# Performance work log

Measured on AMD Instinct MI355X. Metric: run time of the kernel, lower is better.

## Reference

```python
import jax, jax.numpy as jnp
import numpy as np

B, L, D = 8, 1024, 768
H, W, Dd = 16, 16, 4          # token grid, H*W*Dd == L
N, R, K = 16, 48, 4           # d_state, dt_rank, d_conv
EPS = 1e-5


def _physical_pos_embed(batch_params, has_velocity):
    # physical coords [B, L, 3]: (distance, angle, velocity/time)
    h_idx = jnp.arange(H, dtype=jnp.float32)[None, :, None, None]
    w_idx = jnp.arange(W, dtype=jnp.float32)[None, None, :, None]
    d_idx = jnp.arange(Dd, dtype=jnp.float32)[None, None, None, :]
    rres = batch_params[:, 0][:, None, None, None]
    ares = batch_params[:, 1][:, None, None, None]
    vres = batch_params[:, 2][:, None, None, None]
    zero = jnp.zeros((1, H, W, Dd), jnp.float32)
    dist = h_idx * rres + zero
    ang = (w_idx - W / 2) * ares + zero
    vel = jnp.where(has_velocity[:, None, None, None],
                    (d_idx - Dd / 2) * vres, d_idx * vres) + zero
    coords = jnp.stack([dist, ang, vel], axis=-1).reshape(B, L, 3)
    mx = coords.max(axis=1, keepdims=True)
    mn = coords.min(axis=1, keepdims=True)
    rng = mx - mn
    rng = jnp.where(rng > 0, rng, jnp.ones_like(rng))
    coords = (coords - mn) / rng
    # sincos embed: D/3 = 256 dims per coord (even -> pure sin/cos)
    fdim = D // 3
    omega = jnp.arange(fdim // 2, dtype=jnp.float32) / (fdim / 2.0)
    omega = 1.0 / (10000.0 ** omega)                      # [128]
    out = jnp.einsum('blc,f->blcf', coords, omega)        # [B,L,3,128]
    emb = jnp.concatenate([jnp.sin(out), jnp.cos(out)], axis=-1)  # [B,L,3,256]
    return emb.reshape(B, L, D)


def _rmsnorm(x, w):
    return x * jax.lax.rsqrt(jnp.mean(x * x, axis=-1, keepdims=True) + EPS) * w


def _mamba(h, in_proj_w, in_proj_b, conv_w, conv_b, x_proj_w,
           dt_proj_w, dt_proj_b, A_log, D_param, out_proj_w, out_proj_b):
    xz = h @ in_proj_w.T + in_proj_b                      # [B,L,2D]
    x_in, z = xz[..., :D], xz[..., D:]
    # causal depthwise conv1d, kernel K
    xp = jnp.pad(x_in, ((0, 0), (K - 1, 0), (0, 0)))
    x_conv = sum(xp[:, k:k + L, :] * conv_w[:, 0, k] for k in range(K))
    x_conv = jax.nn.silu(x_conv + conv_b)
    x_dbl = x_conv @ x_proj_w.T                           # [B,L,R+2N]
    dt, Bm, Cm = x_dbl[..., :R], x_dbl[..., R:R + N], x_dbl[..., R + N:]
    dt = jax.nn.softplus(dt @ dt_proj_w.T + dt_proj_b)    # [B,L,D]
    A = -jnp.exp(A_log)                                   # [D,N]
    dA = jnp.exp(dt[..., None] * A)                       # [B,L,D,N]
    dBx = dt[..., None] * Bm[:, :, None, :] * x_conv[..., None]

    def step(hst, inp):
        dA_t, dBx_t, C_t = inp
        hst = dA_t * hst + dBx_t                          # [B,D,N]
        y_t = jnp.einsum('bdn,bn->bd', hst, C_t)
        return hst, y_t

    h0 = jnp.zeros((B, D, N), x_in.dtype)
    _, ys = jax.lax.scan(step, h0, (dA.transpose(1, 0, 2, 3),
                                    dBx.transpose(1, 0, 2, 3),
                                    Cm.transpose(1, 0, 2)))
    y = ys.transpose(1, 0, 2) + D_param * x_conv          # [B,L,D]
    y = y * jax.nn.silu(z)
    return y @ out_proj_w.T + out_proj_b


def reference(x, batch_params, has_velocity, norm_w, in_proj_w, in_proj_b,
              conv_w, conv_b, x_proj_w, dt_proj_w, dt_proj_b, A_log,
              D_param, out_proj_w, out_proj_b):
    pos = _physical_pos_embed(batch_params, has_velocity)
    residual = x + pos                                    # ARBlock residual
    hidden = _rmsnorm(residual, norm_w)
    hidden = _mamba(hidden, in_proj_w, in_proj_b, conv_w, conv_b, x_proj_w,
                    dt_proj_w, dt_proj_b, A_log, D_param,
                    out_proj_w, out_proj_b)
    return hidden + residual


def setup_inputs():
    key = jax.random.key(0)
    ks = jax.random.split(key, 12)
    s = 0.02
    return {
        'x': jax.random.normal(ks[0], (B, L, D), jnp.float32),
        'batch_params': jax.random.uniform(ks[1], (B, 4), jnp.float32, 0.01, 1.0),
        'has_velocity': jax.random.randint(ks[2], (B,), 0, 2) > 0,
        'norm_w': jnp.ones((D,), jnp.float32),
        'in_proj_w': jax.random.normal(ks[3], (2 * D, D), jnp.float32) * s,
        'in_proj_b': jnp.zeros((2 * D,), jnp.float32),
        'conv_w': jax.random.normal(ks[4], (D, 1, K), jnp.float32) * 0.3,
        'conv_b': jnp.zeros((D,), jnp.float32),
        'x_proj_w': jax.random.normal(ks[5], (R + 2 * N, D), jnp.float32) * s,
        'dt_proj_w': jax.random.normal(ks[6], (D, R), jnp.float32) * s,
        'dt_proj_b': jax.random.normal(ks[7], (D,), jnp.float32) * 0.1,
        'A_log': jnp.log(jax.random.uniform(ks[8], (D, N), jnp.float32, 1.0, 16.0)),
        'D_param': jnp.ones((D,), jnp.float32),
        'out_proj_w': jax.random.normal(ks[9], (D, D), jnp.float32) * s,
        'out_proj_b': jnp.zeros((D,), jnp.float32),
    }
```

## Files before the change

### kernel.cpp

```cpp
#include <hip/hip_runtime.h>
#include <math.h>

#define BB 8
#define LL 1024
#define DD 768
#define NNs 16
#define RR 48

typedef __attribute__((ext_vector_type(8))) short bf16x8;
typedef __attribute__((ext_vector_type(4))) float f32x4;

__device__ __forceinline__ float silu_f(float v) { return v / (1.0f + __expf(-v)); }

__device__ __forceinline__ short f2bf(float f) {
    union { float f; unsigned u; } v; v.f = f;
    unsigned r = (v.u + 0x7fffu + ((v.u >> 16) & 1u)) >> 16;
    return (short)r;
}

__device__ __forceinline__ float exp2_fast(float x) {
    float r;
    asm("v_exp_f32 %0, %1" : "=v"(r) : "v"(x));
    return r;
}

__device__ __forceinline__ void async16(const void* g, void* l) {
    __builtin_amdgcn_global_load_lds((const __attribute__((address_space(1))) void*)g,
                                     (__attribute__((address_space(3))) void*)l,
                                     16, 0, 0);
}

__global__ __launch_bounds__(256) void k_cvt2(const float* __restrict__ s1,
                                              short* __restrict__ d1, int n1,
                                              const float* __restrict__ s2,
                                              short* __restrict__ d2, int n2) {
    int i = blockIdx.x * 256 + threadIdx.x;
    if (i < n1) {
        float4 v = ((const float4*)s1)[i];
        short4 o = { f2bf(v.x), f2bf(v.y), f2bf(v.z), f2bf(v.w) };
        ((short4*)d1)[i] = o;
    } else {
        int j = i - n1;
        if (j < n2) {
            float4 v = ((const float4*)s2)[j];
            short4 o = { f2bf(v.x), f2bf(v.y), f2bf(v.z), f2bf(v.w) };
            ((short4*)d2)[j] = o;
        }
    }
}

__global__ __launch_bounds__(256) void k_pos_rms(const float* __restrict__ x,
                                                 const float* __restrict__ norm_w,
                                                 float* __restrict__ res,
                                                 short* __restrict__ hidb) {
    int row = blockIdx.x;
    int l = row & (LL - 1);
    int d3 = l & 3;
    int w = (l >> 2) & 15;
    int h = l >> 6;
    float coord[3] = { h * (1.0f / 15.0f), w * (1.0f / 15.0f), d3 * (1.0f / 3.0f) };
    const float LOG1E4 = 9.210340371976184f;
    int t = threadIdx.x;
    float r[3];
    float s = 0.0f;
#pragma unroll
    for (int i = 0; i < 3; i++) {
        int j = t + i * 256;
        int c = j >> 8;
        int fp = j & 255;
        int f = fp & 127;
        float omega = __expf(-(f * (1.0f / 128.0f)) * LOG1E4);
        float arg = coord[c] * omega;
        float pv = (fp < 128) ? __sinf(arg) : __cosf(arg);
        float rv = x[(size_t)row * DD + j] + pv;
        r[i] = rv;
        s += rv * rv;
    }
#pragma unroll
    for (int off = 32; off; off >>= 1) s += __shfl_xor(s, off, 64);
    __shared__ float ls[4];
    if ((t & 63) == 0) ls[t >> 6] = s;
    __syncthreads();
    s = ls[0] + ls[1] + ls[2] + ls[3];
    float rs = rsqrtf(s * (1.0f / DD) + 1e-5f);
#pragma unroll
    for (int i = 0; i < 3; i++) {
        int j = t + i * 256;
        res[(size_t)row * DD + j] = r[i];
        hidb[(size_t)row * DD + j] = f2bf(r[i] * rs * norm_w[j]);
    }
}

template <int EPI, bool AF32>
__global__ __launch_bounds__(256) void gemm_mfma(const void* __restrict__ Ap,
                                                 const short* __restrict__ Bw,
                                                 int Kd,
                                                 const float* __restrict__ bias,
                                                 const float* __restrict__ resid,
                                                 float* __restrict__ C0,
                                                 float* __restrict__ C1) {
    __shared__ short As[4096];
    __shared__ short Bs[4096];
    int m0 = blockIdx.y * 128;
    int n0 = blockIdx.x * 128;
    int tid = threadIdx.x;
    int lane = tid & 63, wave = tid >> 6;
    int q = lane >> 4, r = lane & 15;
    int wm = wave >> 1, wn = wave & 1;

    const size_t Kb = (size_t)Kd * 2;
    const char* gB0 = (const char*)Bw + (size_t)(n0 + wave * 16 + r) * Kb + q * 16;
    const char* gB1 = gB0 + 64 * Kb;
    char* lB0 = (char*)Bs + wave * 1024;
    char* lB1 = lB0 + 4096;
    const char* gA0 = nullptr; const char* gA1 = nullptr;
    char* lA0 = nullptr; char* lA1 = nullptr;
    if (!AF32) {
        gA0 = (const char*)Ap + (size_t)(m0 + wave * 16 + r) * Kb + q * 16;
        gA1 = gA0 + 64 * Kb;
        lA0 = (char*)As + wave * 1024;
        lA1 = lA0 + 4096;
    }

    f32x4 acc[4][4] = {};

    for (int k0 = 0; k0 < Kd; k0 += 32) {
        if (AF32) {
            const float* Af = (const float*)Ap;
#pragma unroll
            for (int p = 0; p < 2; p++) {
                int m = m0 + (p * 4 + wave) * 16 + r;
                const float* src = Af + (size_t)m * Kd + k0 + q * 8;
                float4 v0 = *(const float4*)src;
                float4 v1 = *(const float4*)(src + 4);
                bf16x8 pk;
                pk[0] = f2bf(v0.x); pk[1] = f2bf(v0.y);
                pk[2] = f2bf(v0.z); pk[3] = f2bf(v0.w);
                pk[4] = f2bf(v1.x); pk[5] = f2bf(v1.y);
                pk[6] = f2bf(v1.z); pk[7] = f2bf(v1.w);
                *(bf16x8*)&As[p * 2048 + wave * 512 + lane * 8] = pk;
            }
        } else {
            async16(gA0, lA0); async16(gA1, lA1);
            gA0 += 64; gA1 += 64;
        }
        async16(gB0, lB0); async16(gB1, lB1);
        gB0 += 64; gB1 += 64;
        __syncthreads();
        bf16x8 af[4], bf[4];
#pragma unroll
        for (int a = 0; a < 4; a++)
            af[a] = *(const bf16x8*)&As[((wm * 4 + a) * 64 + q * 16 + r) * 8];
#pragma unroll
        for (int b = 0; b < 4; b++)
            bf[b] = *(const bf16x8*)&Bs[((wn * 4 + b) * 64 + q * 16 + r) * 8];
#pragma unroll
        for (int a = 0; a < 4; a++)
#pragma unroll
            for (int b = 0; b < 4; b++)
                acc[a][b] = __builtin_amdgcn_mfma_f32_16x16x32_bf16(
                    af[a], bf[b], acc[a][b], 0, 0, 0);
        __syncthreads();
    }

#pragma unroll
    for (int a = 0; a < 4; a++) {
        int mrow = m0 + (wm * 4 + a) * 16 + q * 4;
#pragma unroll
        for (int b = 0; b < 4; b++) {
            int ncol = n0 + (wn * 4 + b) * 16 + r;
            float bb = bias[ncol];
            if (EPI == 1) {
                float* dst = (ncol < DD) ? (C0 + (size_t)mrow * DD + ncol)
                                         : (C1 + (size_t)mrow * DD + (ncol - DD));
#pragma unroll
                for (int e = 0; e < 4; e++)
                    dst[(size_t)e * DD] = acc[a][b][e] + bb;
            } else {
#pragma unroll
                for (int e = 0; e < 4; e++) {
                    size_t idx = (size_t)(mrow + e) * DD + ncol;
                    C0[idx] = acc[a][b][e] + bb + resid[idx];
                }
            }
        }
    }
}

template <int MODE>
__global__ __launch_bounds__(256) void gemm_nt(const float* __restrict__ A, int lda,
                                               const float* __restrict__ Bw, int ldb,
                                               int N, int Kd,
                                               const float* __restrict__ bias,
                                               float* __restrict__ C0, int ldc) {
    __shared__ __align__(16) float As[16][68];
    __shared__ __align__(16) float Bs[16][68];
    int m0 = blockIdx.y * 64;
    int n0 = blockIdx.x * 64;
    int t = threadIdx.x;
    int tx = t & 15, ty = t >> 4;
    int ar = t >> 2;
    int ak = (t & 3) * 4;
    float acc[4][4] = {};
    for (int k0 = 0; k0 < Kd; k0 += 16) {
        float4 av = *(const float4*)(A + (size_t)(m0 + ar) * lda + k0 + ak);
        int brow = n0 + ar;
        if (brow >= N) brow = N - 1;
        float4 bv = *(const float4*)(Bw + (size_t)brow * ldb + k0 + ak);
        As[ak + 0][ar] = av.x; As[ak + 1][ar] = av.y;
        As[ak + 2][ar] = av.z; As[ak + 3][ar] = av.w;
        Bs[ak + 0][ar] = bv.x; Bs[ak + 1][ar] = bv.y;
        Bs[ak + 2][ar] = bv.z; Bs[ak + 3][ar] = bv.w;
        __syncthreads();
#pragma unroll
        for (int kk = 0; kk < 16; kk++) {
            float4 a4 = *(const float4*)&As[kk][ty * 4];
            float4 b4 = *(const float4*)&Bs[kk][tx * 4];
            float aa[4] = { a4.x, a4.y, a4.z, a4.w };
            float bb[4] = { b4.x, b4.y, b4.z, b4.w };
#pragma unroll
            for (int i = 0; i < 4; i++)
#pragma unroll
                for (int j = 0; j < 4; j++) acc[i][j] += aa[i] * bb[j];
        }
        __syncthreads();
    }
    if (MODE == 0) {
#pragma unroll
        for (int i = 0; i < 4; i++) {
            int m = m0 + ty * 4 + i;
#pragma unroll
            for (int j = 0; j < 4; j++) {
                int n = n0 + tx * 4 + j;
                if (n < N) C0[(size_t)m * ldc + n] = acc[i][j];
            }
        }
    } else {
        float4 bi = *(const float4*)(bias + n0 + tx * 4);
        float bl[4] = { bi.x, bi.y, bi.z, bi.w };
#pragma unroll
        for (int i = 0; i < 4; i++) {
            int m = m0 + ty * 4 + i;
            float v[4];
#pragma unroll
            for (int j = 0; j < 4; j++) {
                float u = acc[i][j] + bl[j];
                v[j] = (u > 20.0f) ? u : log1pf(__expf(u));
            }
            float4 o = { v[0], v[1], v[2], v[3] };
            *(float4*)(C0 + (size_t)m * DD + n0 + tx * 4) = o;
        }
    }
}

__global__ __launch_bounds__(256) void k_conv(const float* __restrict__ xin,
                                              const float* __restrict__ cw,
                                              const float* __restrict__ cb,
                                              float* __restrict__ xc) {
    size_t gid = (size_t)blockIdx.x * 256 + threadIdx.x;
    int d = (int)(gid % DD);
    int bt = (int)(gid / DD);
    int tt = bt & (LL - 1);
    float4 w = ((const float4*)cw)[d];
    const float* p = xin + (size_t)bt * DD + d;
    float acc = cb[d];
    if (tt >= 3) acc += p[-3 * DD] * w.x;
    if (tt >= 2) acc += p[-2 * DD] * w.y;
    if (tt >= 1) acc += p[-1 * DD] * w.z;
    acc += p[0] * w.w;
    xc[gid] = silu_f(acc);
}

__global__ __launch_bounds__(256, 3) void k_scan(const float* __restrict__ dtf,
                                                 const float* __restrict__ xc,
                                                 const float* __restrict__ xdbl,
                                                 const float* __restrict__ A_log,
                                                 const float* __restrict__ Dp,
                                                 float* __restrict__ zy) {
    __shared__ float Pl[32 * 8 * 16];
    __shared__ float Sl[32 * 8 * 16];
    int bid = blockIdx.x;
    int xcd = bid & 7;
    int v = bid >> 3;
    int dtile = xcd * 12 + (v % 12);
    int b = v / 12;
    int d0 = dtile * 8;
    int tid = threadIdx.x;
    int dl = tid & 7;
    int c = tid >> 3;
    int d = d0 + dl;

    const float LOG2E = 1.4426950408889634f;
    float Ac[16];
    {
        const float4* al = (const float4*)(A_log + d * NNs);
#pragma unroll
        for (int i = 0; i < 4; i++) {
            float4 v4 = al[i];
            Ac[i * 4 + 0] = -__expf(v4.x) * LOG2E;
            Ac[i * 4 + 1] = -__expf(v4.y) * LOG2E;
            Ac[i * 4 + 2] = -__expf(v4.z) * LOG2E;
            Ac[i * 4 + 3] = -__expf(v4.w) * LOG2E;
        }
    }
    size_t rb = ((size_t)(b * LL + c * 32)) * DD + d;
    const float* dtp = dtf + rb;
    const float* xcp = xc + rb;
    float* zp = zy + rb;
    const float* xrow = xdbl + ((size_t)(b * LL + c * 32)) * 80 + RR;

    float S[16];
#pragma unroll
    for (int n = 0; n < 16; n++) S[n] = 0.0f;
    float dtsum = 0.0f;
    {
        float dt0 = dtp[0], xc0 = xcp[0];
        float dt1 = dtp[DD], xc1 = xcp[DD];
        float4 Bb[4];
#pragma unroll
        for (int qq = 0; qq < 4; qq++) Bb[qq] = *(const float4*)(xrow + qq * 4);
        for (int i = 0; i < 32; i++) {
            int i2 = (i + 2 < 32) ? i + 2 : 31;
            int i1 = (i + 1 < 32) ? i + 1 : 31;
            float dt2 = dtp[(size_t)i2 * DD];
            float xc2 = xcp[(size_t)i2 * DD];
            float4 nB[4];
            const float* nBr = xrow + i1 * 80;
#pragma unroll
            for (int qq = 0; qq < 4; qq++) nB[qq] = *(const float4*)(nBr + qq * 4);

            float dx = dt0 * xc0;
            dtsum += dt0;
#pragma unroll
            for (int qq = 0; qq < 4; qq++) {
                float bl[4] = { Bb[qq].x, Bb[qq].y, Bb[qq].z, Bb[qq].w };
#pragma unroll
                for (int j = 0; j < 4; j++) {
                    int n = qq * 4 + j;
                    float e = exp2_fast(dt0 * Ac[n]);
                    S[n] = e * S[n] + dx * bl[j];
                }
            }
            dt0 = dt1; dt1 = dt2;
            xc0 = xc1; xc1 = xc2;
#pragma unroll
            for (int qq = 0; qq < 4; qq++) Bb[qq] = nB[qq];
        }
    }
    {
        float* pw = &Pl[(c * 8 + dl) * 16];
        float* sw = &Sl[(c * 8 + dl) * 16];
#pragma unroll
        for (int qq = 0; qq < 4; qq++) {
            float4 pv = { exp2_fast(Ac[qq * 4 + 0] * dtsum),
                          exp2_fast(Ac[qq * 4 + 1] * dtsum),
                          exp2_fast(Ac[qq * 4 + 2] * dtsum),
                          exp2_fast(Ac[qq * 4 + 3] * dtsum) };
            float4 sv = { S[qq * 4], S[qq * 4 + 1], S[qq * 4 + 2], S[qq * 4 + 3] };
            *(float4*)(pw + qq * 4) = pv;
            *(float4*)(sw + qq * 4) = sv;
        }
    }
    __syncthreads();
    if (tid < 128) {
        int d2 = tid >> 4, n2 = tid & 15;
        float hh = 0.0f;
#pragma unroll
        for (int cc = 0; cc < 32; cc++) {
            int idx = (cc * 8 + d2) * 16 + n2;
            float Pv = Pl[idx], Sv = Sl[idx];
            Pl[idx] = hh;
            hh = Pv * hh + Sv;
        }
    }
    __syncthreads();
    float h[16];
    {
        const float* hr = &Pl[(c * 8 + dl) * 16];
#pragma unroll
        for (int qq = 0; qq < 4; qq++) {
            float4 v4 = *(const float4*)(hr + qq * 4);
            h[qq * 4] = v4.x; h[qq * 4 + 1] = v4.y;
            h[qq * 4 + 2] = v4.z; h[qq * 4 + 3] = v4.w;
        }
    }
    float Dv = Dp[d];
    {
        float dt0 = dtp[0], xc0 = xcp[0], zv0 = zp[0];
        float dt1 = dtp[DD], xc1 = xcp[DD], zv1 = zp[DD];
        float4 Bb[4], Cc[4];
#pragma unroll
        for (int qq = 0; qq < 4; qq++) {
            Bb[qq] = *(const float4*)(xrow + qq * 4);
            Cc[qq] = *(const float4*)(xrow + 16 + qq * 4);
        }
        for (int i = 0; i < 32; i++) {
            int i2 = (i + 2 < 32) ? i + 2 : 31;
            int i1 = (i + 1 < 32) ? i + 1 : 31;
            float dt2 = dtp[(size_t)i2 * DD];
            float xc2 = xcp[(size_t)i2 * DD];
            float zv2 = zp[(size_t)i2 * DD];
            float4 nB[4], nC[4];
            const float* nBr = xrow + i1 * 80;
#pragma unroll
            for (int qq = 0; qq < 4; qq++) {
                nB[qq] = *(const float4*)(nBr + qq * 4);
                nC[qq] = *(const float4*)(nBr + 16 + qq * 4);
            }
            float dx = dt0 * xc0;
            float y = Dv * xc0;
#pragma unroll
            for (int qq = 0; qq < 4; qq++) {
                float bl[4] = { Bb[qq].x, Bb[qq].y, Bb[qq].z, Bb[qq].w };
                float cl[4] = { Cc[qq].x, Cc[qq].y, Cc[qq].z, Cc[qq].w };
#pragma unroll
                for (int j = 0; j < 4; j++) {
                    int n = qq * 4 + j;
                    float e = exp2_fast(dt0 * Ac[n]);
                    h[n] = e * h[n] + dx * bl[j];
                    y += h[n] * cl[j];
                }
            }
            zp[(size_t)i * DD] = y * silu_f(zv0);
            dt0 = dt1; dt1 = dt2;
            xc0 = xc1; xc1 = xc2;
            zv0 = zv1; zv1 = zv2;
#pragma unroll
            for (int qq = 0; qq < 4; qq++) { Bb[qq] = nB[qq]; Cc[qq] = nC[qq]; }
        }
    }
}

extern "C" void kernel_launch(void* const* d_in, const int* in_sizes, int n_in,
                              void* d_out, int out_size, void* d_ws, size_t ws_size,
                              hipStream_t stream) {
    const float* x      = (const float*)d_in[0];
    const float* norm_w = (const float*)d_in[3];
    const float* in_w   = (const float*)d_in[4];
    const float* in_b   = (const float*)d_in[5];
    const float* conv_w = (const float*)d_in[6];
    const float* conv_b = (const float*)d_in[7];
    const float* xp_w   = (const float*)d_in[8];
    const float* dt_w   = (const float*)d_in[9];
    const float* dt_b   = (const float*)d_in[10];
    const float* A_log  = (const float*)d_in[11];
    const float* Dp     = (const float*)d_in[12];
    const float* out_w  = (const float*)d_in[13];
    const float* out_b  = (const float*)d_in[14];
    float* out = (float*)d_out;

    const size_t S = (size_t)BB * LL * DD;
    float* res   = (float*)d_ws;
    float* slotA = res + S;
    float* slotB = slotA + S;
    float* zf    = slotB + S;
    float* xdbl  = zf + S;
    short* inw_b  = (short*)(xdbl + (size_t)BB * LL * 80);
    short* outw_b = inw_b + 1536 * DD;

    short* hidb = (short*)slotA;
    float* xc   = slotA;
    float* xin  = slotB;
    float* dtf  = slotB;

    const int M = BB * LL;

    {
        int n1 = 1536 * DD / 4, n2 = DD * DD / 4;
        k_cvt2<<<(n1 + n2 + 255) / 256, 256, 0, stream>>>(in_w, inw_b, n1,
                                                          out_w, outw_b, n2);
    }

    k_pos_rms<<<M, 256, 0, stream>>>(x, norm_w, res, hidb);

    gemm_mfma<1, false><<<dim3(1536 / 128, M / 128), 256, 0, stream>>>(
        hidb, inw_b, DD, in_b, nullptr, xin, zf);

    k_conv<<<(int)(S / 256), 256, 0, stream>>>(xin, conv_w, conv_b, xc);

    gemm_nt<0><<<dim3(2, M / 64), 256, 0, stream>>>(
        xc, DD, xp_w, DD, RR + 2 * NNs, DD, nullptr, xdbl, 80);

    gemm_nt<2><<<dim3(DD / 64, M / 64), 256, 0, stream>>>(
        xdbl, 80, dt_w, RR, DD, RR, dt_b, dtf, DD);

    k_scan<<<768, 256, 0, stream>>>(dtf, xc, xdbl, A_log, Dp, zf);

    gemm_mfma<3, true><<<dim3(DD / 128, M / 128), 256, 0, stream>>>(
        zf, outw_b, DD, out_b, res, out, nullptr);
}
```

Baseline: 370.1 us.

## Pack scan state math into v_pk_fma and emit bf16 gated output for out_proj

The selective-scan kernel now holds its state as float pairs and updates them with packed fp32 multiply/FMA instructions, which cuts VALU issue count in the inner loops. When the workspace is large enough, the scan also writes the gated output directly as bf16 into a new buffer. The output-projection GEMM then reads bf16 A operands and skips its fp32-to-bf16 conversion path. This halves the write and read traffic between the two kernels. The cost is a rounding change in the output, which the old path already applied inside the GEMM, and a larger workspace requirement with an fp32 fallback.

Measured after the change: 358.9 us. -3.0%, faster.

```diff
diff --git a/kernel.cpp b/kernel.cpp
--- a/kernel.cpp
+++ b/kernel.cpp
@@ -9,6 +9,7 @@
 
 typedef __attribute__((ext_vector_type(8))) short bf16x8;
 typedef __attribute__((ext_vector_type(4))) float f32x4;
+typedef __attribute__((ext_vector_type(2))) float f32x2;
 
 __device__ __forceinline__ float silu_f(float v) { return v / (1.0f + __expf(-v)); }
 
@@ -22,6 +23,17 @@
     float r;
     asm("v_exp_f32 %0, %1" : "=v"(r) : "v"(x));
     return r;
+}
+
+__device__ __forceinline__ f32x2 pk_fma(f32x2 a, f32x2 b, f32x2 c) {
+    f32x2 d;
+    asm("v_pk_fma_f32 %0, %1, %2, %3" : "=v"(d) : "v"(a), "v"(b), "v"(c));
+    return d;
+}
+__device__ __forceinline__ f32x2 pk_mul(f32x2 a, f32x2 b) {
+    f32x2 d;
+    asm("v_pk_mul_f32 %0, %1, %2" : "=v"(d) : "v"(a), "v"(b));
+    return d;
 }
 
 __device__ __forceinline__ void async16(const void* g, void* l) {
@@ -271,12 +283,14 @@
     xc[gid] = silu_f(acc);
 }
 
+template <bool YB>
 __global__ __launch_bounds__(256, 3) void k_scan(const float* __restrict__ dtf,
                                                  const float* __restrict__ xc,
                                                  const float* __restrict__ xdbl,
                                                  const float* __restrict__ A_log,
                                                  const float* __restrict__ Dp,
-                                                 float* __restrict__ zy) {
+                                                 float* __restrict__ zy,
+                                                 short* __restrict__ yb) {
     __shared__ float Pl[32 * 8 * 16];
     __shared__ float Sl[32 * 8 * 16];
     int bid = blockIdx.x;
@@ -291,27 +305,26 @@
     int d = d0 + dl;
 
     const float LOG2E = 1.4426950408889634f;
-    float Ac[16];
+    f32x2 Ac2[8];
     {
         const float4* al = (const float4*)(A_log + d * NNs);
 #pragma unroll
         for (int i = 0; i < 4; i++) {
             float4 v4 = al[i];
-            Ac[i * 4 + 0] = -__expf(v4.x) * LOG2E;
-            Ac[i * 4 + 1] = -__expf(v4.y) * LOG2E;
-            Ac[i * 4 + 2] = -__expf(v4.z) * LOG2E;
-            Ac[i * 4 + 3] = -__expf(v4.w) * LOG2E;
+            Ac2[i * 2]     = (f32x2){ -__expf(v4.x) * LOG2E, -__expf(v4.y) * LOG2E };
+            Ac2[i * 2 + 1] = (f32x2){ -__expf(v4.z) * LOG2E, -__expf(v4.w) * LOG2E };
         }
     }
     size_t rb = ((size_t)(b * LL + c * 32)) * DD + d;
     const float* dtp = dtf + rb;
     const float* xcp = xc + rb;
     float* zp = zy + rb;
+    short* ybp = yb + rb;
     const float* xrow = xdbl + ((size_t)(b * LL + c * 32)) * 80 + RR;
 
-    float S[16];
-#pragma unroll
-    for (int n = 0; n < 16; n++) S[n] = 0.0f;
+    f32x2 S2[8];
+#pragma unroll
+    for (int k = 0; k < 8; k++) S2[k] = (f32x2){ 0.0f, 0.0f };
     float dtsum = 0.0f;
     {
         float dt0 = dtp[0], xc0 = xcp[0];
@@ -331,15 +344,18 @@
 
             float dx = dt0 * xc0;
             dtsum += dt0;
-#pragma unroll
-            for (int qq = 0; qq < 4; qq++) {
-                float bl[4] = { Bb[qq].x, Bb[qq].y, Bb[qq].z, Bb[qq].w };
-#pragma unroll
-                for (int j = 0; j < 4; j++) {
-                    int n = qq * 4 + j;
-                    float e = exp2_fast(dt0 * Ac[n]);
-                    S[n] = e * S[n] + dx * bl[j];
-                }
+            f32x2 dtp2 = (f32x2){ dt0, dt0 };
+            f32x2 dx2 = (f32x2){ dx, dx };
+#pragma unroll
+            for (int k = 0; k < 8; k++) {
+                float4 qb = Bb[k >> 1];
+                f32x2 bl2 = (k & 1) ? (f32x2){ qb.z, qb.w } : (f32x2){ qb.x, qb.y };
+                f32x2 arg = pk_mul(dtp2, Ac2[k]);
+                f32x2 e2;
+                e2[0] = exp2_fast(arg[0]);
+                e2[1] = exp2_fast(arg[1]);
+                f32x2 dxb = pk_mul(dx2, bl2);
+                S2[k] = pk_fma(e2, S2[k], dxb);
             }
             dt0 = dt1; dt1 = dt2;
             xc0 = xc1; xc1 = xc2;
@@ -351,14 +367,15 @@
         float* pw = &Pl[(c * 8 + dl) * 16];
         float* sw = &Sl[(c * 8 + dl) * 16];
 #pragma unroll
-        for (int qq = 0; qq < 4; qq++) {
-            float4 pv = { exp2_fast(Ac[qq * 4 + 0] * dtsum),
-                          exp2_fast(Ac[qq * 4 + 1] * dtsum),
-                          exp2_fast(Ac[qq * 4 + 2] * dtsum),
-                          exp2_fast(Ac[qq * 4 + 3] * dtsum) };
-            float4 sv = { S[qq * 4], S[qq * 4 + 1], S[qq * 4 + 2], S[qq * 4 + 3] };
-            *(float4*)(pw + qq * 4) = pv;
-            *(float4*)(sw + qq * 4) = sv;
+        for (int q2 = 0; q2 < 4; q2++) {
+            float4 pv = { exp2_fast(Ac2[q2 * 2][0] * dtsum),
+                          exp2_fast(Ac2[q2 * 2][1] * dtsum),
+                          exp2_fast(Ac2[q2 * 2 + 1][0] * dtsum),
+                          exp2_fast(Ac2[q2 * 2 + 1][1] * dtsum) };
+            float4 sv = { S2[q2 * 2][0], S2[q2 * 2][1],
+                          S2[q2 * 2 + 1][0], S2[q2 * 2 + 1][1] };
+            *(float4*)(pw + q2 * 4) = pv;
+            *(float4*)(sw + q2 * 4) = sv;
         }
     }
     __syncthreads();
@@ -374,14 +391,14 @@
         }
     }
     __syncthreads();
-    float h[16];
+    f32x2 h2[8];
     {
         const float* hr = &Pl[(c * 8 + dl) * 16];
 #pragma unroll
-        for (int qq = 0; qq < 4; qq++) {
-            float4 v4 = *(const float4*)(hr + qq * 4);
-            h[qq * 4] = v4.x; h[qq * 4 + 1] = v4.y;
-            h[qq * 4 + 2] = v4.z; h[qq * 4 + 3] = v4.w;
+        for (int q2 = 0; q2 < 4; q2++) {
+            float4 v4 = *(const float4*)(hr + q2 * 4);
+            h2[q2 * 2]     = (f32x2){ v4.x, v4.y };
+            h2[q2 * 2 + 1] = (f32x2){ v4.z, v4.w };
         }
     }
     float Dv = Dp[d];
@@ -408,20 +425,27 @@
                 nC[qq] = *(const float4*)(nBr + 16 + qq * 4);
             }
             float dx = dt0 * xc0;
-            float y = Dv * xc0;
-#pragma unroll
-            for (int qq = 0; qq < 4; qq++) {
-                float bl[4] = { Bb[qq].x, Bb[qq].y, Bb[qq].z, Bb[qq].w };
-                float cl[4] = { Cc[qq].x, Cc[qq].y, Cc[qq].z, Cc[qq].w };
-#pragma unroll
-                for (int j = 0; j < 4; j++) {
-                    int n = qq * 4 + j;
-                    float e = exp2_fast(dt0 * Ac[n]);
-                    h[n] = e * h[n] + dx * bl[j];
-                    y += h[n] * cl[j];
-                }
-            }
-            zp[(size_t)i * DD] = y * silu_f(zv0);
+            f32x2 dtp2 = (f32x2){ dt0, dt0 };
+            f32x2 dx2 = (f32x2){ dx, dx };
+            f32x2 y2 = (f32x2){ Dv * xc0, 0.0f };
+#pragma unroll
+            for (int k = 0; k < 8; k++) {
+                float4 qb = Bb[k >> 1];
+                float4 qc = Cc[k >> 1];
+                f32x2 bl2 = (k & 1) ? (f32x2){ qb.z, qb.w } : (f32x2){ qb.x, qb.y };
+                f32x2 cl2 = (k & 1) ? (f32x2){ qc.z, qc.w } : (f32x2){ qc.x, qc.y };
+                f32x2 arg = pk_mul(dtp2, Ac2[k]);
+                f32x2 e2;
+                e2[0] = exp2_fast(arg[0]);
+                e2[1] = exp2_fast(arg[1]);
+                f32x2 dxb = pk_mul(dx2, bl2);
+                h2[k] = pk_fma(e2, h2[k], dxb);
+                y2 = pk_fma(h2[k], cl2, y2);
+            }
+            float y = y2[0] + y2[1];
+            float gated = y * silu_f(zv0);
+            if (YB) ybp[(size_t)i * DD] = f2bf(gated);
+            else    zp[(size_t)i * DD] = gated;
             dt0 = dt1; dt1 = dt2;
             xc0 = xc1; xc1 = xc2;
             zv0 = zv1; zv1 = zv2;
@@ -457,6 +481,7 @@
     float* xdbl  = zf + S;
     short* inw_b  = (short*)(xdbl + (size_t)BB * LL * 80);
     short* outw_b = inw_b + 1536 * DD;
+    short* ybf    = outw_b + DD * DD;
 
     short* hidb = (short*)slotA;
     float* xc   = slotA;
@@ -465,6 +490,9 @@
 
     const int M = BB * LL;
 
+    size_t need = (size_t)((char*)(ybf + S) - (char*)d_ws);
+    bool useYB = ws_size >= need;
+
     {
         int n1 = 1536 * DD / 4, n2 = DD * DD / 4;
         k_cvt2<<<(n1 + n2 + 255) / 256, 256, 0, stream>>>(in_w, inw_b, n1,
@@ -484,8 +512,13 @@
     gemm_nt<2><<<dim3(DD / 64, M / 64), 256, 0, stream>>>(
         xdbl, 80, dt_w, RR, DD, RR, dt_b, dtf, DD);
 
-    k_scan<<<768, 256, 0, stream>>>(dtf, xc, xdbl, A_log, Dp, zf);
-
-    gemm_mfma<3, true><<<dim3(DD / 128, M / 128), 256, 0, stream>>>(
-        zf, outw_b, DD, out_b, res, out, nullptr);
-}
+    if (useYB) {
+        k_scan<true><<<768, 256, 0, stream>>>(dtf, xc, xdbl, A_log, Dp, zf, ybf);
+        gemm_mfma<3, false><<<dim3(DD / 128, M / 128), 256, 0, stream>>>(
+            ybf, outw_b, DD, out_b, res, out, nullptr);
+    } else {
+        k_scan<false><<<768, 256, 0, stream>>>(dtf, xc, xdbl, A_log, Dp, zf, ybf);
+        gemm_mfma<3, true><<<dim3(DD / 128, M / 128), 256, 0, stream>>>(
+            zf, outw_b, DD, out_b, res, out, nullptr);
+    }
+}
```
